# Performance work log

Hardware: AMD Instinct MI355X
Metric: run time of the kernel (lower is better)

## Reference

```python
import jax, jax.numpy as jnp
import numpy as np

B, S, D_IN, D_OUT = 2, 2048, 4096, 4096


def setup_inputs() -> dict:
    key = jax.random.key(0)
    kx, kw, kb = jax.random.split(key, 3)
    x = jax.random.normal(kx, (B, S, D_IN), dtype=jnp.float32)
    weight = jax.random.normal(kw, (D_OUT, D_IN), dtype=jnp.float32)
    bias = jax.random.normal(kb, (D_OUT,), dtype=jnp.float32)
    return {"x": x, "weight": weight, "bias": bias}


def reference(x, weight, bias):
    # FdaBinary forward is simply sign(); linear with binarized weight.
    w_bin = jnp.sign(weight)  # [D_OUT, D_IN], values in {-1, 0, +1}
    # F.linear: x @ w.T + b
    out = jnp.einsum("bsd,od->bso", x, w_bin) + bias
    return out
```

## Files before the change

kernel.cpp:

```cpp
#include <hip/hip_runtime.h>
#include <hip/hip_bf16.h>
#include <stdint.h>
#include <stddef.h>

#define M_DIM 4096
#define N_DIM 4096
#define K_DIM 4096
#define BM 256
#define BN 256
#define BK 64
#define NKT (K_DIM / BK)
#define BKB (BK * 2)
#define RSTRIDE ((size_t)64 * K_DIM * 2)

typedef __bf16 bf16;
typedef __attribute__((ext_vector_type(4))) __bf16 bf16x4;
typedef __attribute__((ext_vector_type(8))) __bf16 bf16x8;
typedef __attribute__((ext_vector_type(4))) float f32x4;

__global__ __launch_bounds__(256) void prep_kernel(const float* __restrict__ x,
                                                   const float* __restrict__ w,
                                                   bf16* __restrict__ xb,
                                                   bf16* __restrict__ wb) {
    const int idx = blockIdx.x * 256 + threadIdx.x;
    float4 xv = ((const float4*)x)[idx];
    bf16x4 xo;
    xo[0] = (bf16)xv.x; xo[1] = (bf16)xv.y; xo[2] = (bf16)xv.z; xo[3] = (bf16)xv.w;
    ((bf16x4*)xb)[idx] = xo;

    float4 wv = ((const float4*)w)[idx];
    bf16x4 wo;
    wo[0] = (bf16)((wv.x > 0.f) ? 1.f : ((wv.x < 0.f) ? -1.f : 0.f));
    wo[1] = (bf16)((wv.y > 0.f) ? 1.f : ((wv.y < 0.f) ? -1.f : 0.f));
    wo[2] = (bf16)((wv.z > 0.f) ? 1.f : ((wv.z < 0.f) ? -1.f : 0.f));
    wo[3] = (bf16)((wv.w > 0.f) ? 1.f : ((wv.w < 0.f) ? -1.f : 0.f));
    ((bf16x4*)wb)[idx] = wo;
}

__device__ __forceinline__ void load_lds16(const void* g, void* l) {
    __builtin_amdgcn_global_load_lds(
        (const __attribute__((address_space(1))) void*)g,
        (__attribute__((address_space(3))) void*)l, 16, 0, 0);
}

__global__ __launch_bounds__(512, 2) void gemm_bin_kernel(const bf16* __restrict__ A,
                                                          const bf16* __restrict__ Bw,
                                                          const float* __restrict__ bias,
                                                          float* __restrict__ C) {
    __shared__ __align__(16) bf16 As[2][BM * BK];
    __shared__ __align__(16) bf16 Bs[2][BM * BK];

    const int tid  = threadIdx.x;
    const int lane = tid & 63;
    const int wave = tid >> 6;
    const int wm   = wave >> 2;
    const int wn   = wave & 3;

    const int tileM = blockIdx.y * BM;
    const int tileN = blockIdx.x * BN;

    const int rowInC = lane >> 3;
    const int q_src  = (lane & 7) ^ rowInC;
    const char* aSrc = (const char*)A  + ((size_t)(tileM + wave * 8 + rowInC) * K_DIM + q_src * 8) * 2;
    const char* bSrc = (const char*)Bw + ((size_t)(tileN + wave * 8 + rowInC) * K_DIM + q_src * 8) * 2;

#define STAGE_A(B_, R_, KOFF_) load_lds16(aSrc + (size_t)(R_) * RSTRIDE + (KOFF_), \
                                          &As[B_][((R_) * 64 + wave * 8) * BK])
#define STAGE_B(B_, R_, KOFF_) load_lds16(bSrc + (size_t)(R_) * RSTRIDE + (KOFF_), \
                                          &Bs[B_][((R_) * 64 + wave * 8) * BK])

    f32x4 acc[8][4];
#pragma unroll
    for (int i = 0; i < 8; ++i)
#pragma unroll
        for (int j = 0; j < 4; ++j)
            acc[i][j] = (f32x4){0.f, 0.f, 0.f, 0.f};

    bf16x8 bfrA[4][2];
    bf16x8 bfrB[4][2];

    const int l15 = lane & 15;
    const int qf  = lane >> 4;
    const int fragRowA = wm * 128 + l15;
    const int fragRowB = wn * 64 + l15;
    const int s0 = (0 + qf) ^ (l15 & 7);
    const int s1 = (4 + qf) ^ (l15 & 7);

#define PREF_AF(B_, P_) \
    _Pragma("unroll") \
    for (int ii = 0; ii < 2; ++ii) { \
        af[ii][0] = *(const bf16x8*)&As[B_][(fragRowA + (2 * (P_) + ii) * 16) * BK + s0 * 8]; \
        af[ii][1] = *(const bf16x8*)&As[B_][(fragRowA + (2 * (P_) + ii) * 16) * BK + s1 * 8]; \
    }

#define READ_BN(DST_, BSRC_) \
    _Pragma("unroll") \
    for (int j = 0; j < 4; ++j) { \
        DST_[j][0] = *(const bf16x8*)&Bs[BSRC_][(fragRowB + j * 16) * BK + s0 * 8]; \
        DST_[j][1] = *(const bf16x8*)&Bs[BSRC_][(fragRowB + j * 16) * BK + s1 * 8]; \
    }

#define MFMA16(P_, BU_) \
    _Pragma("unroll") \
    for (int ii = 0; ii < 2; ++ii) \
        _Pragma("unroll") \
        for (int j = 0; j < 4; ++j) { \
            acc[2 * (P_) + ii][j] = __builtin_amdgcn_mfma_f32_16x16x32_bf16(af[ii][0], BU_[j][0], acc[2 * (P_) + ii][j], 0, 0, 0); \
            acc[2 * (P_) + ii][j] = __builtin_amdgcn_mfma_f32_16x16x32_bf16(af[ii][1], BU_[j][1], acc[2 * (P_) + ii][j], 0, 0, 0); \
        }

#define VMCNT8 asm volatile("s_waitcnt vmcnt(8)" ::: "memory")
#define VMCNT6 asm volatile("s_waitcnt vmcnt(6)" ::: "memory")
#define BAR    __builtin_amdgcn_s_barrier()
#define SCHED0 __builtin_amdgcn_sched_barrier(0)
#define PRIO1  __builtin_amdgcn_s_setprio(1)
#define PRIO0  __builtin_amdgcn_s_setprio(0)

#define KTILE(B_, BU_, BN_, K1_, K2_) do { \
        { bf16x8 af[2][2]; \
          PREF_AF(B_, 0); \
          STAGE_A((B_) ^ 1, 1, K1_); STAGE_A((B_) ^ 1, 3, K1_); \
          BAR; PRIO1; MFMA16(0, BU_); PRIO0; VMCNT8; BAR; SCHED0; } \
        { bf16x8 af[2][2]; \
          PREF_AF(B_, 1); \
          STAGE_B(B_, 0, K2_); STAGE_B(B_, 1, K2_); \
          BAR; PRIO1; MFMA16(1, BU_); PRIO0; BAR; SCHED0; } \
        { bf16x8 af[2][2]; \
          PREF_AF(B_, 2); \
          STAGE_B(B_, 2, K2_); STAGE_B(B_, 3, K2_); \
          BAR; PRIO1; MFMA16(2, BU_); PRIO0; VMCNT6; BAR; SCHED0; } \
        { bf16x8 af[2][2]; \
          PREF_AF(B_, 3); \
          SCHED0; \
          READ_BN(BN_, (B_) ^ 1); \
          STAGE_A(B_, 0, K2_); STAGE_A(B_, 2, K2_); \
          BAR; PRIO1; MFMA16(3, BU_); PRIO0; BAR; SCHED0; } \
    } while (0)

    STAGE_B(0, 0, 0);   STAGE_B(0, 1, 0);   STAGE_B(0, 2, 0);   STAGE_B(0, 3, 0);
    STAGE_A(0, 0, 0);   STAGE_A(0, 2, 0);   STAGE_A(0, 1, 0);   STAGE_A(0, 3, 0);
    STAGE_B(1, 0, BKB); STAGE_B(1, 1, BKB); STAGE_B(1, 2, BKB); STAGE_B(1, 3, BKB);
    STAGE_A(1, 0, BKB); STAGE_A(1, 2, BKB);
    VMCNT6;
    BAR;
    SCHED0;
    READ_BN(bfrA, 0);

    for (int kt = 0; kt < NKT; kt += 2) {
        const int k1a = (kt + 1) * BKB;
        const int k2a = (kt + 2 < NKT) ? (kt + 2) * BKB : 0;
        KTILE(0, bfrA, bfrB, k1a, k2a);
        const int k2b = (kt + 3 < NKT) ? (kt + 3) * BKB : 0;
        KTILE(1, bfrB, bfrA, k2a, k2b);
    }

#pragma unroll
    for (int j = 0; j < 4; ++j) {
        const int col = tileN + wn * 64 + j * 16 + l15;
        const float bv = bias[col];
#pragma unroll
        for (int i = 0; i < 8; ++i) {
            const int row0 = tileM + wm * 128 + i * 16 + (qf << 2);
#pragma unroll
            for (int rr = 0; rr < 4; ++rr) {
                C[(size_t)(row0 + rr) * N_DIM + col] = acc[i][j][rr] + bv;
            }
        }
    }

#undef STAGE_A
#undef STAGE_B
#undef PREF_AF
#undef READ_BN
#undef MFMA16
#undef VMCNT8
#undef VMCNT6
#undef BAR
#undef SCHED0
#undef PRIO1
#undef PRIO0
#undef KTILE
}

extern "C" void kernel_launch(void* const* d_in, const int* in_sizes, int n_in,
                              void* d_out, int out_size, void* d_ws, size_t ws_size,
                              hipStream_t stream) {
    const float* x    = (const float*)d_in[0];
    const float* w    = (const float*)d_in[1];
    const float* bias = (const float*)d_in[2];
    float* out        = (float*)d_out;

    const int nElem = M_DIM * K_DIM;
    bf16* xb = (bf16*)d_ws;
    bf16* wb = xb + (size_t)nElem;

    prep_kernel<<<nElem / 4 / 256, 256, 0, stream>>>(x, w, xb, wb);

    dim3 grid(N_DIM / BN, M_DIM / BM);
    gemm_bin_kernel<<<grid, 512, 0, stream>>>(xb, wb, bias, out);
}
```

Measured before the change: 294.3 us.

## Switch GEMM to 32x32x16 MFMA and two-phase K-tile schedule

Result: faster. 285.8 us (-2.9%).

```diff
diff --git a/kernel.cpp b/kernel.cpp
--- a/kernel.cpp
+++ b/kernel.cpp
@@ -17,6 +17,7 @@
 typedef __attribute__((ext_vector_type(4))) __bf16 bf16x4;
 typedef __attribute__((ext_vector_type(8))) __bf16 bf16x8;
 typedef __attribute__((ext_vector_type(4))) float f32x4;
+typedef __attribute__((ext_vector_type(16))) float f32x16;
 
 __global__ __launch_bounds__(256) void prep_kernel(const float* __restrict__ x,
                                                    const float* __restrict__ w,
@@ -69,72 +70,64 @@
 #define STAGE_B(B_, R_, KOFF_) load_lds16(bSrc + (size_t)(R_) * RSTRIDE + (KOFF_), \
                                           &Bs[B_][((R_) * 64 + wave * 8) * BK])
 
-    f32x4 acc[8][4];
+    f32x16 acc[4][2];
 #pragma unroll
-    for (int i = 0; i < 8; ++i)
+    for (int i = 0; i < 4; ++i)
 #pragma unroll
-        for (int j = 0; j < 4; ++j)
-            acc[i][j] = (f32x4){0.f, 0.f, 0.f, 0.f};
+        for (int j = 0; j < 2; ++j)
+            acc[i][j] = (f32x16){0.f,0.f,0.f,0.f,0.f,0.f,0.f,0.f,
+                                 0.f,0.f,0.f,0.f,0.f,0.f,0.f,0.f};
 
-    bf16x8 bfrA[4][2];
-    bf16x8 bfrB[4][2];
+    bf16x8 bfr[2][4];
 
-    const int l15 = lane & 15;
-    const int qf  = lane >> 4;
-    const int fragRowA = wm * 128 + l15;
-    const int fragRowB = wn * 64 + l15;
-    const int s0 = (0 + qf) ^ (l15 & 7);
-    const int s1 = (4 + qf) ^ (l15 & 7);
+    const int l31 = lane & 31;
+    const int hi  = lane >> 5;
+    const int sl7 = lane & 7;
 
-#define PREF_AF(B_, P_) \
-    _Pragma("unroll") \
-    for (int ii = 0; ii < 2; ++ii) { \
-        af[ii][0] = *(const bf16x8*)&As[B_][(fragRowA + (2 * (P_) + ii) * 16) * BK + s0 * 8]; \
-        af[ii][1] = *(const bf16x8*)&As[B_][(fragRowA + (2 * (P_) + ii) * 16) * BK + s1 * 8]; \
-    }
+#define ASLOT(KS_) ((((KS_) * 2 + hi) ^ sl7) * 8)
 
-#define READ_BN(DST_, BSRC_) \
-    _Pragma("unroll") \
-    for (int j = 0; j < 4; ++j) { \
-        DST_[j][0] = *(const bf16x8*)&Bs[BSRC_][(fragRowB + j * 16) * BK + s0 * 8]; \
-        DST_[j][1] = *(const bf16x8*)&Bs[BSRC_][(fragRowB + j * 16) * BK + s1 * 8]; \
-    }
-
-#define MFMA16(P_, BU_) \
+#define READ_A(B_, P_) \
     _Pragma("unroll") \
     for (int ii = 0; ii < 2; ++ii) \
         _Pragma("unroll") \
-        for (int j = 0; j < 4; ++j) { \
-            acc[2 * (P_) + ii][j] = __builtin_amdgcn_mfma_f32_16x16x32_bf16(af[ii][0], BU_[j][0], acc[2 * (P_) + ii][j], 0, 0, 0); \
-            acc[2 * (P_) + ii][j] = __builtin_amdgcn_mfma_f32_16x16x32_bf16(af[ii][1], BU_[j][1], acc[2 * (P_) + ii][j], 0, 0, 0); \
-        }
+        for (int ks = 0; ks < 4; ++ks) \
+            af[ii][ks] = *(const bf16x8*)&As[B_][(wm * 128 + (P_) * 64 + ii * 32 + l31) * BK + ASLOT(ks)];
 
-#define VMCNT8 asm volatile("s_waitcnt vmcnt(8)" ::: "memory")
+#define READ_B(B_) \
+    _Pragma("unroll") \
+    for (int j = 0; j < 2; ++j) \
+        _Pragma("unroll") \
+        for (int ks = 0; ks < 4; ++ks) \
+            bfr[j][ks] = *(const bf16x8*)&Bs[B_][(wn * 64 + j * 32 + l31) * BK + ASLOT(ks)];
+
+#define MFMA32(P_) \
+    _Pragma("unroll") \
+    for (int ks = 0; ks < 4; ++ks) \
+        _Pragma("unroll") \
+        for (int ii = 0; ii < 2; ++ii) \
+            _Pragma("unroll") \
+            for (int j = 0; j < 2; ++j) \
+                acc[2 * (P_) + ii][j] = __builtin_amdgcn_mfma_f32_32x32x16_bf16( \
+                    af[ii][ks], bfr[j][ks], acc[2 * (P_) + ii][j], 0, 0, 0);
+
 #define VMCNT6 asm volatile("s_waitcnt vmcnt(6)" ::: "memory")
 #define BAR    __builtin_amdgcn_s_barrier()
 #define SCHED0 __builtin_amdgcn_sched_barrier(0)
 #define PRIO1  __builtin_amdgcn_s_setprio(1)
 #define PRIO0  __builtin_amdgcn_s_setprio(0)
 
-#define KTILE(B_, BU_, BN_, K1_, K2_) do { \
-        { bf16x8 af[2][2]; \
-          PREF_AF(B_, 0); \
+#define KTILE(B_, K1_, K2_) do { \
+        { bf16x8 af[2][4]; \
+          READ_B(B_); \
+          READ_A(B_, 0); \
           STAGE_A((B_) ^ 1, 1, K1_); STAGE_A((B_) ^ 1, 3, K1_); \
-          BAR; PRIO1; MFMA16(0, BU_); PRIO0; VMCNT8; BAR; SCHED0; } \
-        { bf16x8 af[2][2]; \
-          PREF_AF(B_, 1); \
+          BAR; PRIO1; MFMA32(0); PRIO0; BAR; SCHED0; } \
+        { bf16x8 af[2][4]; \
+          READ_A(B_, 1); \
           STAGE_B(B_, 0, K2_); STAGE_B(B_, 1, K2_); \
-          BAR; PRIO1; MFMA16(1, BU_); PRIO0; BAR; SCHED0; } \
-        { bf16x8 af[2][2]; \
-          PREF_AF(B_, 2); \
           STAGE_B(B_, 2, K2_); STAGE_B(B_, 3, K2_); \
-          BAR; PRIO1; MFMA16(2, BU_); PRIO0; VMCNT6; BAR; SCHED0; } \
-        { bf16x8 af[2][2]; \
-          PREF_AF(B_, 3); \
-          SCHED0; \
-          READ_BN(BN_, (B_) ^ 1); \
           STAGE_A(B_, 0, K2_); STAGE_A(B_, 2, K2_); \
-          BAR; PRIO1; MFMA16(3, BU_); PRIO0; BAR; SCHED0; } \
+          BAR; PRIO1; MFMA32(1); PRIO0; VMCNT6; BAR; SCHED0; } \
     } while (0)
 
     STAGE_B(0, 0, 0);   STAGE_B(0, 1, 0);   STAGE_B(0, 2, 0);   STAGE_B(0, 3, 0);
@@ -144,36 +137,36 @@
     VMCNT6;
     BAR;
     SCHED0;
-    READ_BN(bfrA, 0);
 
     for (int kt = 0; kt < NKT; kt += 2) {
         const int k1a = (kt + 1) * BKB;
         const int k2a = (kt + 2 < NKT) ? (kt + 2) * BKB : 0;
-        KTILE(0, bfrA, bfrB, k1a, k2a);
+        KTILE(0, k1a, k2a);
         const int k2b = (kt + 3 < NKT) ? (kt + 3) * BKB : 0;
-        KTILE(1, bfrB, bfrA, k2a, k2b);
+        KTILE(1, k2a, k2b);
     }
 
 #pragma unroll
-    for (int j = 0; j < 4; ++j) {
-        const int col = tileN + wn * 64 + j * 16 + l15;
+    for (int j = 0; j < 2; ++j) {
+        const int col = tileN + wn * 64 + j * 32 + l31;
         const float bv = bias[col];
 #pragma unroll
-        for (int i = 0; i < 8; ++i) {
-            const int row0 = tileM + wm * 128 + i * 16 + (qf << 2);
+        for (int i = 0; i < 4; ++i) {
+            const int rowBase = tileM + wm * 128 + i * 32 + hi * 4;
 #pragma unroll
-            for (int rr = 0; rr < 4; ++rr) {
-                C[(size_t)(row0 + rr) * N_DIM + col] = acc[i][j][rr] + bv;
+            for (int reg = 0; reg < 16; ++reg) {
+                const int row = rowBase + (reg & 3) + 8 * (reg >> 2);
+                C[(size_t)row * N_DIM + col] = acc[i][j][reg] + bv;
             }
         }
     }
 
 #undef STAGE_A
 #undef STAGE_B
-#undef PREF_AF
-#undef READ_BN
-#undef MFMA16
-#undef VMCNT8
+#undef ASLOT
+#undef READ_A
+#undef READ_B
+#undef MFMA32
 #undef VMCNT6
 #undef BAR
 #undef SCHED0
```
